# Optimization experiments

Measured on AMD Instinct MI355X. Metric: run time of the kernel, lower is better.

Reference implementation:

```python
import jax, jax.numpy as jnp
import numpy as np

HID = 2048        # hidden_size
STATE = 128       # ssm state size N
HEADS = 64
HEADDIM = 64
GROUPS = 1
K = 4             # conv kernel
INTER = 4096      # expand * hidden_size == HEADS * HEADDIM
CONV_DIM = INTER + 2 * GROUPS * STATE   # 4352
PROJ = INTER + CONV_DIM + HEADS         # 8512
EPS = 1e-5


def setup_inputs() -> dict:
    ks = jax.random.split(jax.random.key(0), 8)
    hidden_states = jax.random.normal(ks[0], (2, 2048, HID), dtype=jnp.float32)
    norm_weight = jnp.ones((HID,), jnp.float32)
    in_proj_w = jax.random.normal(ks[1], (PROJ, HID), jnp.float32) * 0.02
    conv_w = jax.random.normal(ks[2], (CONV_DIM, 1, K), jnp.float32) * 0.1
    conv_b = jax.random.normal(ks[3], (CONV_DIM,), jnp.float32) * 0.02
    dt_bias = jax.random.normal(ks[4], (HEADS,), jnp.float32) * 0.5
    A_log = jnp.log(jnp.arange(1, HEADS + 1, dtype=jnp.float32))
    D = jnp.ones((HEADS,), jnp.float32)
    gate_norm_weight = jnp.ones((INTER,), jnp.float32)
    out_proj_w = jax.random.normal(ks[5], (HID, INTER), jnp.float32) * 0.02
    return {"hidden_states": hidden_states, "norm_weight": norm_weight,
            "in_proj_w": in_proj_w, "conv_w": conv_w, "conv_b": conv_b,
            "dt_bias": dt_bias, "A_log": A_log, "D": D,
            "gate_norm_weight": gate_norm_weight, "out_proj_w": out_proj_w}


def _rmsnorm(x, w, eps):
    v = jnp.mean(jnp.square(x.astype(jnp.float32)), axis=-1, keepdims=True)
    return (x * jax.lax.rsqrt(v + eps)) * w


def _mamba2_block(hidden_states, norm_weight, in_proj_w, conv_w, conv_b,
                  dt_bias, A_log, D, gate_norm_weight, out_proj_w):
    b, s, _ = hidden_states.shape
    residual = hidden_states.astype(jnp.float32)  # residual_in_fp32
    x = _rmsnorm(hidden_states, norm_weight, EPS)

    proj = x @ in_proj_w.T                                  # [b,s,PROJ]
    gate, xBC, dt = jnp.split(proj, [INTER, INTER + CONV_DIM], axis=-1)

    # causal depthwise conv1d over channels, then SiLU
    xBC_t = jnp.swapaxes(xBC, 1, 2)                          # [b,C,s]
    conv = jax.lax.conv_general_dilated(
        xBC_t, conv_w, window_strides=(1,), padding=[(K - 1, 0)],
        dimension_numbers=("NCH", "OIH", "NCH"), feature_group_count=CONV_DIM)
    xBC = jax.nn.silu(jnp.swapaxes(conv + conv_b[None, :, None], 1, 2))

    xs, B, C = jnp.split(xBC, [INTER, INTER + GROUPS * STATE], axis=-1)
    hg = HEADS // GROUPS
    xs = xs.reshape(b, s, GROUPS, hg, HEADDIM)
    B = B.reshape(b, s, GROUPS, STATE)
    C = C.reshape(b, s, GROUPS, STATE)

    dt = jax.nn.softplus(dt + dt_bias).reshape(b, s, GROUPS, hg)  # [b,s,g,hg]
    A = -jnp.exp(A_log).reshape(GROUPS, hg)
    dA = jnp.exp(dt * A)                                     # [b,s,g,hg]
    dtx = dt[..., None] * xs                                  # [b,s,g,hg,p]

    def step(state, inp):
        dA_t, dtx_t, B_t, C_t = inp
        # state: [b,g,hg,p,n]
        state = state * dA_t[..., None, None] + jnp.einsum("bghp,bgn->bghpn", dtx_t, B_t)
        y_t = jnp.einsum("bghpn,bgn->bghp", state, C_t)
        return state, y_t

    mv = lambda a: jnp.moveaxis(a, 1, 0)  # time-major for scan
    state0 = jnp.zeros((b, GROUPS, hg, HEADDIM, STATE), jnp.float32)
    _, y = jax.lax.scan(step, state0, (mv(dA), mv(dtx), mv(B), mv(C)))
    y = jnp.moveaxis(y, 0, 1)                                 # [b,s,g,hg,p]
    y = y + D.reshape(GROUPS, hg)[..., None] * xs             # skip term
    y = y.reshape(b, s, INTER)

    # gated RMSNorm then output projection
    y = _rmsnorm(y * jax.nn.silu(gate), gate_norm_weight, EPS)
    out = y @ out_proj_w.T
    return residual + out


def reference(hidden_states, norm_weight, in_proj_w, conv_w, conv_b,
              dt_bias, A_log, D, gate_norm_weight, out_proj_w):
    return _mamba2_block(hidden_states, norm_weight, in_proj_w, conv_w, conv_b,
                         dt_bias, A_log, D, gate_norm_weight, out_proj_w)
```

## Files before the change

### kernel.cpp

```cpp
#include <hip/hip_runtime.h>
#include <math.h>

#define HID      2048
#define STATE    128
#define HEADS    64
#define HEADDIM  64
#define INTER    4096
#define CONV_DIM 4352
#define PROJ     8512
#define NBATCH   2
#define SEQ      2048
#define BS       (NBATCH*SEQ)
#define EPS      1e-5f
#define YN_COL   4160

typedef __attribute__((ext_vector_type(8))) short short8;
typedef __attribute__((ext_vector_type(4))) float f32x4;

__device__ inline unsigned short f2bf(float f) {
  union { float f; unsigned int u; } v; v.f = f;
  unsigned int r = v.u + 0x7fffu + ((v.u >> 16) & 1u);
  return (unsigned short)(r >> 16);
}
__device__ inline float bf2f(unsigned short b) {
  union { unsigned int u; float f; } v; v.u = ((unsigned int)b) << 16;
  return v.f;
}

__global__ __launch_bounds__(256)
void cast_bf16_kernel(const float4* __restrict__ src, ushort4* __restrict__ dst, int n4) {
  int i = blockIdx.x * 256 + threadIdx.x;
  if (i >= n4) return;
  float4 v = src[i];
  ushort4 o;
  o.x = f2bf(v.x); o.y = f2bf(v.y); o.z = f2bf(v.z); o.w = f2bf(v.w);
  dst[i] = o;
}

__global__ __launch_bounds__(256)
void rmsnorm_in_kernel(const float* __restrict__ x, const float* __restrict__ w,
                       unsigned short* __restrict__ xn) {
  int row = blockIdx.x;
  int t = threadIdx.x;
  const float* xr = x + (size_t)row * HID;
  float4 a = ((const float4*)xr)[t];
  float4 b = ((const float4*)xr)[t + 256];
  float ss = a.x*a.x + a.y*a.y + a.z*a.z + a.w*a.w
           + b.x*b.x + b.y*b.y + b.z*b.z + b.w*b.w;
  for (int o = 32; o > 0; o >>= 1) ss += __shfl_down(ss, o);
  __shared__ float red[4];
  __shared__ float scl;
  if ((t & 63) == 0) red[t >> 6] = ss;
  __syncthreads();
  if (t == 0) scl = rsqrtf((red[0]+red[1]+red[2]+red[3]) / (float)HID + EPS);
  __syncthreads();
  float s = scl;
  float4 w0 = ((const float4*)w)[t];
  float4 w1 = ((const float4*)w)[t + 256];
  ushort4 o0, o1;
  o0.x = f2bf(a.x*s*w0.x); o0.y = f2bf(a.y*s*w0.y); o0.z = f2bf(a.z*s*w0.z); o0.w = f2bf(a.w*s*w0.w);
  o1.x = f2bf(b.x*s*w1.x); o1.y = f2bf(b.y*s*w1.y); o1.z = f2bf(b.z*s*w1.z); o1.w = f2bf(b.w*s*w1.w);
  ushort4* dst = (ushort4*)(xn + (size_t)row * HID);
  dst[t] = o0;
  dst[t + 256] = o1;
}


__device__ __forceinline__ void stage_half(const unsigned short* __restrict__ G, int ld,
                                           int row0, int rmax, int kt,
                                           unsigned short* lbase, int half, int t) {
  const int w = t >> 6;
#pragma unroll
  for (int it = 0; it < 2; ++it) {
    int id = it * 512 + t;
    int rl = id >> 3;
    int sl = id & 7;
    int grow = row0 + half * 128 + rl;
    if (grow > rmax) grow = rmax;
    const unsigned short* g = G + (size_t)grow * ld + kt * 64 + ((sl ^ (rl & 7)) << 3);
    unsigned short* l = lbase + half * (128 * 64) + (it * 512 + w * 64) * 8;
    __builtin_amdgcn_global_load_lds((const __attribute__((address_space(1))) void*)g,
                                     (__attribute__((address_space(3))) void*)l, 16, 0, 0);
  }
}

#define VMW2 asm volatile("s_waitcnt vmcnt(2)" ::: "memory")

#define PHASE(BUF, MH, NH, RA, RB, STG, VMW_)                                        \
  {                                                                                  \
    const unsigned short* bufA = lds + (BUF)*24576;                                  \
    const unsigned short* bufB = lds + (BUF)*24576 + 16384;                          \
    if (RA) {                                                                        \
      _Pragma("unroll")                                                              \
      for (int ml = 0; ml < 2; ++ml) {                                               \
        _Pragma("unroll")                                                            \
        for (int kk = 0; kk < 2; ++kk) {                                             \
          const int r = wr*64 + (MH)*32 + ml*16 + tq;                                \
          aR[ml][kk] = *(const short8*)(bufA + r*64 + (((kk<<2)|quad)^(r&7))*8);     \
        }                                                                            \
      }                                                                              \
    }                                                                                \
    if (RB) {                                                                        \
      _Pragma("unroll")                                                              \
      for (int nl = 0; nl < 2; ++nl) {                                               \
        _Pragma("unroll")                                                            \
        for (int kk = 0; kk < 2; ++kk) {                                             \
          const int r = wc*64 + (NH)*32 + nl*16 + tq;                                \
          bR[NH][nl][kk] = *(const short8*)(bufB + r*64 + (((kk<<2)|quad)^(r&7))*8); \
        }                                                                            \
      }                                                                              \
    }                                                                                \
    STG;                                                                             \
    __builtin_amdgcn_s_barrier();                                                    \
    asm volatile("s_waitcnt lgkmcnt(0)" ::: "memory");                               \
    __builtin_amdgcn_sched_barrier(0);                                               \
    __builtin_amdgcn_s_setprio(1);                                                   \
    _Pragma("unroll")                                                                \
    for (int ml = 0; ml < 2; ++ml) {                                                 \
      _Pragma("unroll")                                                              \
      for (int nl = 0; nl < 2; ++nl) {                                               \
        _Pragma("unroll")                                                            \
        for (int kk = 0; kk < 2; ++kk) {                                             \
          acc[(MH)*2+ml][(NH)*2+nl] = __builtin_amdgcn_mfma_f32_16x16x32_bf16(       \
              aR[ml][kk], bR[NH][nl][kk], acc[(MH)*2+ml][(NH)*2+nl], 0, 0, 0);       \
        }                                                                            \
      }                                                                              \
    }                                                                                \
    __builtin_amdgcn_s_setprio(0);                                                   \
    VMW_;                                                                            \
    __builtin_amdgcn_s_barrier();                                                    \
  }

__global__ __launch_bounds__(512, 1)
void gemm128n_kernel(const unsigned short* __restrict__ A, int lda,
                     const unsigned short* __restrict__ B,
                     float* __restrict__ Cf, unsigned short* __restrict__ Cb, int ldc,
                     int M, int N, int Kd, const float* __restrict__ residual) {
  __shared__ unsigned short lds[49152];
  const int t = threadIdx.x;
  const int lane = t & 63;
  const int quad = lane >> 4;
  const int tq = lane & 15;
  const int w = t >> 6;
  const int wr = w >> 1;
  const int wc = w & 1;

  const int Mtiles = M >> 8;
  const int Ntiles = (N + 127) >> 7;
  const int nwg = (int)gridDim.x;
  const int cpx = nwg >> 3;
  const int bid = (int)blockIdx.x;
  const int sw = (bid & 7) * cpx + (bid >> 3);
  const int NBfull = Ntiles & ~7;
  int m0, n0;
  if (sw < Mtiles * NBfull) {
    int brick = sw >> 5;
    int inner = sw & 31;
    int bm = brick % (Mtiles >> 2);
    int bn = brick / (Mtiles >> 2);
    m0 = (bm * 4 + (inner & 3)) << 8;
    n0 = (bn * 8 + (inner >> 2)) << 7;
  } else {
    int r = sw - Mtiles * NBfull;
    m0 = (r % Mtiles) << 8;
    n0 = (NBfull + r / Mtiles) << 7;
  }

  f32x4 acc[4][4];
#pragma unroll
  for (int i = 0; i < 4; ++i)
#pragma unroll
    for (int j = 0; j < 4; ++j) acc[i][j] = (f32x4){0.f, 0.f, 0.f, 0.f};

  short8 aR[2][2];
  short8 bR[2][2][2];

  unsigned short* A0 = lds;
  unsigned short* B0 = lds + 16384;
  unsigned short* A1 = lds + 24576;
  unsigned short* B1 = lds + 24576 + 16384;

  const int kIters = Kd >> 6;
  const int nIter  = kIters >> 1;

  stage_half(A, lda, m0, M - 1, 0, A0, 0, t);
  stage_half(A, lda, m0, M - 1, 0, A0, 1, t);
  stage_half(B, Kd,  n0, N - 1, 0, B0, 0, t);
  stage_half(A, lda, m0, M - 1, 1, A1, 0, t);
  VMW2;
  __builtin_amdgcn_s_barrier();

  for (int i = 0; i < nIter; ++i) {
    const int k1 = 2 * i + 1;
    int k2 = 2 * i + 2; if (k2 > kIters - 1) k2 = kIters - 1;
    int k3 = 2 * i + 3; if (k3 > kIters - 1) k3 = kIters - 1;
    PHASE(0, 0, 0, 1, 1, stage_half(A, lda, m0, M - 1, k1, A1, 1, t), ((void)0))
    PHASE(0, 0, 1, 0, 1, stage_half(B, Kd,  n0, N - 1, k1, B1, 0, t), ((void)0))
    PHASE(0, 1, 1, 1, 0, ((void)0), ((void)0))
    PHASE(0, 1, 0, 0, 0, stage_half(A, lda, m0, M - 1, k2, A0, 0, t), VMW2)
    PHASE(1, 0, 0, 1, 1, stage_half(A, lda, m0, M - 1, k2, A0, 1, t), ((void)0))
    PHASE(1, 0, 1, 0, 1, stage_half(B, Kd,  n0, N - 1, k2, B0, 0, t), ((void)0))
    PHASE(1, 1, 1, 1, 0, ((void)0), ((void)0))
    PHASE(1, 1, 0, 0, 0, stage_half(A, lda, m0, M - 1, k3, A1, 0, t), VMW2)
  }
  asm volatile("s_waitcnt vmcnt(0)" ::: "memory");

#pragma unroll
  for (int mf = 0; mf < 4; ++mf) {
    const int rowb = m0 + wr * 64 + mf * 16 + quad * 4;
#pragma unroll
    for (int nf = 0; nf < 4; ++nf) {
      const int col = n0 + wc * 64 + nf * 16 + tq;
      if (col < N) {
        if (Cb) {
#pragma unroll
          for (int r = 0; r < 4; ++r)
            Cb[(size_t)(rowb + r) * ldc + col] = f2bf(acc[mf][nf][r]);
        } else {
#pragma unroll
          for (int r = 0; r < 4; ++r) {
            size_t idx = (size_t)(rowb + r) * N + col;
            float v = acc[mf][nf][r];
            if (residual) v += residual[idx];
            Cf[idx] = v;
          }
        }
      }
    }
  }
}

#define CONV_BC 128
#define CONV_BS 64
#define CXS 136

__global__ __launch_bounds__(256)
void conv_dt_kernel(const unsigned short* __restrict__ proj, const float* __restrict__ cw,
                    const float* __restrict__ cb, const float* __restrict__ dtb,
                    const float* __restrict__ A_log,
                    unsigned short* __restrict__ convo, float2* __restrict__ dts) {
  const int NCB = CONV_DIM / CONV_BC;
  const int NCONVB = NCB * (BS / CONV_BS);
  int blk = blockIdx.x;
  int t = threadIdx.x;
  if (blk < NCONVB) {
    __shared__ unsigned short xs[67 * CXS];
    int cblk = blk % NCB;
    int rblk = blk / NCB;
    int ch0 = cblk * CONV_BC;
    int rs0 = rblk * CONV_BS;
    int s0 = rs0 & (SEQ - 1);
    const int c8 = t & 15;
    const int co = c8 * 8;
    float cwr[4][8], cbr[8];
#pragma unroll
    for (int e = 0; e < 8; e++) {
      cbr[e] = cb[ch0 + co + e];
#pragma unroll
      for (int k = 0; k < 4; k++) cwr[k][e] = cw[(ch0 + co + e) * 4 + k];
    }
    for (int i = t; i < 67 * 16; i += 256) {
      int row = i >> 4, sl = i & 15;
      short8 v;
      if (s0 == 0 && row < 3) v = (short8){0,0,0,0,0,0,0,0};
      else v = *(const short8*)&proj[(size_t)(rs0 - 3 + row) * PROJ + INTER + ch0 + sl * 8];
      *(short8*)&xs[row * CXS + sl * 8] = v;
    }
    __syncthreads();
#pragma unroll
    for (int it = 0; it < 4; ++it) {
      int r = (t >> 4) + it * 16;
      float acc[8];
#pragma unroll
      for (int e = 0; e < 8; e++) acc[e] = cbr[e];
#pragma unroll
      for (int k = 0; k < 4; k++) {
        short8 v = *(const short8*)&xs[(r + k) * CXS + co];
#pragma unroll
        for (int e = 0; e < 8; e++) acc[e] += bf2f((unsigned short)v[e]) * cwr[k][e];
      }
      short8 o;
#pragma unroll
      for (int e = 0; e < 8; e++) {
        float a = acc[e];
        o[e] = (short)f2bf(a / (1.f + expf(-a)));
      }
      *(short8*)&convo[(size_t)(rs0 + r) * CONV_DIM + ch0 + co] = o;
    }
  } else {
    int k = (blk - NCONVB) * 256 + t;
    if (k < BS * HEADS) {
      int h  = k & 63;
      int rs = k >> 6;
      float x = bf2f(proj[(size_t)rs * PROJ + INTER + CONV_DIM + h]) + dtb[h];
      float dt = (x > 20.f) ? x : log1pf(expf(x));
      float Ah = -expf(A_log[h]);
      dts[k] = make_float2(dt, dt * Ah);
    }
  }
}

#define LCH 64
#define CST 136
#define TST 72

__global__ __launch_bounds__(512)
void ssd_scan_kernel(const unsigned short* __restrict__ convo, const float2* __restrict__ dts,
                     unsigned short* __restrict__ yp) {
  __shared__ unsigned short Cst[64 * CST];
  __shared__ unsigned short Bst[64 * CST];
  __shared__ unsigned short Btt[128 * TST];
  __shared__ unsigned short xtT[32 * TST];
  __shared__ unsigned short Msh[64 * TST];
  __shared__ unsigned short Sb[2][32 * CST];
  __shared__ float dtaL[64], dtvL[64];

  const int ph = blockIdx.x & 1;
  const int h  = (blockIdx.x >> 1) & 63;
  const int b  = blockIdx.x >> 7;
  const int t  = threadIdx.x;
  const int wv = t >> 6;
  const int lane = t & 63;
  const int quad = lane >> 4;
  const int tq   = lane & 15;
  const size_t row0 = (size_t)b * SEQ;
  const int xcol = h * 64 + ph * 32;

  for (int i = t; i < 32 * CST; i += 512) Sb[0][i] = 0;

  f32x4 s_acc[4];
#pragma unroll
  for (int c = 0; c < 4; c++) s_acc[c] = (f32x4){0.f, 0.f, 0.f, 0.f};
  const int pt  = wv & 1;
  const int ntb = ((wv >> 1) & 1) * 4;

  short8 vb_r[2], vc_r[2]; ushort4 vx_r; float2 dv_r = make_float2(0.f, 0.f);
  {
#pragma unroll
    for (int it = 0; it < 2; ++it) {
      int id = t + 512 * it;
      int row = id >> 4, cc = id & 15;
      size_t g = (row0 + row) * CONV_DIM + INTER;
      vb_r[it] = *(const short8*)&convo[g + cc * 8];
      vc_r[it] = *(const short8*)&convo[g + STATE + cc * 8];
    }
    int row = t >> 3, c = t & 7;
    vx_r = *(const ushort4*)&convo[(row0 + row) * CONV_DIM + xcol + c * 4];
    if (t < 64) dv_r = dts[((row0 + t) << 6) + h];
  }

  int pp = 0;
  for (int c0 = 0; c0 < SEQ; c0 += LCH, pp ^= 1) {
    __syncthreads();
#pragma unroll
    for (int it = 0; it < 2; ++it) {
      int id = t + 512 * it;
      int row = id >> 4, cc = id & 15;
      *(short8*)&Bst[row * CST + cc * 8] = vb_r[it];
      *(short8*)&Cst[row * CST + cc * 8] = vc_r[it];
#pragma unroll
      for (int e = 0; e < 8; e++)
        Btt[(cc * 8 + e) * TST + row] = (unsigned short)vb_r[it][e];
    }
    {
      int row = t >> 3, c = t & 7;
      xtT[(c * 4 + 0) * TST + row] = vx_r.x;
      xtT[(c * 4 + 1) * TST + row] = vx_r.y;
      xtT[(c * 4 + 2) * TST + row] = vx_r.z;
      xtT[(c * 4 + 3) * TST + row] = vx_r.w;
    }
    if (t < 64) { dtvL[t] = dv_r.x; dtaL[t] = dv_r.y; }
    __syncthreads();

    if (c0 + LCH < SEQ) {
#pragma unroll
      for (int it = 0; it < 2; ++it) {
        int id = t + 512 * it;
        int row = id >> 4, cc = id & 15;
        size_t g = (row0 + c0 + LCH + row) * CONV_DIM + INTER;
        vb_r[it] = *(const short8*)&convo[g + cc * 8];
        vc_r[it] = *(const short8*)&convo[g + STATE + cc * 8];
      }
      int row = t >> 3, c = t & 7;
      vx_r = *(const ushort4*)&convo[(row0 + c0 + LCH + row) * CONV_DIM + xcol + c * 4];
      if (t < 64) dv_r = dts[((row0 + c0 + LCH + t) << 6) + h];
    }

    float v = dtaL[lane];
#pragma unroll
    for (int off = 1; off < 64; off <<= 1) {
      float u = __shfl_up(v, off);
      if (lane >= off) v += u;
    }
    float tot = __shfl(v, 63);

    if (wv < 4) {
      short8 afC[4];
#pragma unroll
      for (int kt = 0; kt < 4; kt++)
        afC[kt] = *(const short8*)&Cst[(16 * wv + tq) * CST + kt * 32 + quad * 8];
      f32x4 g_acc[4];
#pragma unroll
      for (int nj = 0; nj < 4; nj++) g_acc[nj] = (f32x4){0.f, 0.f, 0.f, 0.f};
#pragma unroll
      for (int kt = 0; kt < 4; kt++) {
#pragma unroll
        for (int nj = 0; nj < 4; nj++) {
          short8 bfr = *(const short8*)&Bst[(16 * nj + tq) * CST + kt * 32 + quad * 8];
          g_acc[nj] = __builtin_amdgcn_mfma_f32_16x16x32_bf16(afC[kt], bfr, g_acc[nj], 0, 0, 0);
        }
      }
      float ci[4], pex[4];
#pragma unroll
      for (int r = 0; r < 4; r++) {
        ci[r] = __shfl(v, 16 * wv + quad * 4 + r);
        pex[r] = expf(ci[r]);
      }
#pragma unroll
      for (int nj = 0; nj < 4; nj++) {
        int j = 16 * nj + tq;
        float cj = __shfl(v, j);
        float dj = dtvL[j];
#pragma unroll
        for (int r = 0; r < 4; r++) {
          int i = 16 * wv + quad * 4 + r;
          float val = (j <= i) ? g_acc[nj][r] * expf(ci[r] - cj) * dj : 0.f;
          Msh[i * TST + j] = f2bf(val);
        }
      }
      f32x4 yac[2];
      yac[0] = (f32x4){0.f, 0.f, 0.f, 0.f};
      yac[1] = (f32x4){0.f, 0.f, 0.f, 0.f};
#pragma unroll
      for (int kt = 0; kt < 4; kt++) {
#pragma unroll
        for (int np = 0; np < 2; np++) {
          short8 bs = *(const short8*)&Sb[pp][(16 * np + tq) * CST + kt * 32 + quad * 8];
          yac[np] = __builtin_amdgcn_mfma_f32_16x16x32_bf16(afC[kt], bs, yac[np], 0, 0, 0);
        }
      }
#pragma unroll
      for (int np = 0; np < 2; np++)
#pragma unroll
        for (int r = 0; r < 4; r++) yac[np][r] *= pex[r];
#pragma unroll
      for (int kt2 = 0; kt2 < 2; kt2++) {
        short8 am = *(const short8*)&Msh[(16 * wv + tq) * TST + kt2 * 32 + quad * 8];
#pragma unroll
        for (int np = 0; np < 2; np++) {
          short8 bx = *(const short8*)&xtT[(16 * np + tq) * TST + kt2 * 32 + quad * 8];
          yac[np] = __builtin_amdgcn_mfma_f32_16x16x32_bf16(am, bx, yac[np], 0, 0, 0);
        }
      }
#pragma unroll
      for (int np = 0; np < 2; np++) {
#pragma unroll
        for (int r = 0; r < 4; r++) {
          int i = 16 * wv + quad * 4 + r;
          int p = ph * 32 + 16 * np + tq;
          yp[(row0 + c0 + i) * INTER + h * 64 + p] = f2bf(yac[np][r]);
        }
      }
    } else {
      float ptot = expf(tot);
      short8 ax[2];
#pragma unroll
      for (int kt2 = 0; kt2 < 2; kt2++) {
        short8 xv = *(const short8*)&xtT[(16 * pt + tq) * TST + kt2 * 32 + quad * 8];
#pragma unroll
        for (int e = 0; e < 8; e++) {
          int j = kt2 * 32 + quad * 8 + e;
          float cj = __shfl(v, j);
          float wj = expf(tot - cj) * dtvL[j];
          ax[kt2][e] = (short)f2bf(bf2f((unsigned short)xv[e]) * wj);
        }
      }
#pragma unroll
      for (int c = 0; c < 4; c++)
#pragma unroll
        for (int r = 0; r < 4; r++) s_acc[c][r] *= ptot;
#pragma unroll
      for (int kt2 = 0; kt2 < 2; kt2++) {
#pragma unroll
        for (int c = 0; c < 4; c++) {
          short8 bb = *(const short8*)&Btt[(16 * (ntb + c) + tq) * TST + kt2 * 32 + quad * 8];
          s_acc[c] = __builtin_amdgcn_mfma_f32_16x16x32_bf16(ax[kt2], bb, s_acc[c], 0, 0, 0);
        }
      }
#pragma unroll
      for (int c = 0; c < 4; c++)
#pragma unroll
        for (int r = 0; r < 4; r++) {
          int p = 16 * pt + quad * 4 + r;
          int n = 16 * (ntb + c) + tq;
          Sb[pp ^ 1][p * CST + n] = f2bf(s_acc[c][r]);
        }
    }
  }
}

__global__ __launch_bounds__(256)
void gated_norm_kernel(const unsigned short* __restrict__ yp,
                       const unsigned short* __restrict__ convo, const unsigned short* __restrict__ proj,
                       const float* __restrict__ Dv, const float* __restrict__ gnw,
                       unsigned short* __restrict__ yn) {
  int row = blockIdx.x;
  int t = threadIdx.x;
  __shared__ float red[4];
  __shared__ float scl;
  size_t yo = (size_t)row * INTER;
  size_t co = (size_t)row * CONV_DIM;
  size_t po = (size_t)row * PROJ;
  float vv[16];
  float ss = 0.f;
#pragma unroll
  for (int c = 0; c < 4; c++) {
    int i = t * 4 + c * 1024;
    ushort4 y0 = *(const ushort4*)&yp[yo + i];
    ushort4 xs = *(const ushort4*)&convo[co + i];
    ushort4 g  = *(const ushort4*)&proj[po + i];
    float Dh = Dv[i >> 6];
    float yv[4] = { bf2f(y0.x) + Dh * bf2f(xs.x),
                    bf2f(y0.y) + Dh * bf2f(xs.y),
                    bf2f(y0.z) + Dh * bf2f(xs.z),
                    bf2f(y0.w) + Dh * bf2f(xs.w) };
    float gv[4] = { bf2f(g.x), bf2f(g.y), bf2f(g.z), bf2f(g.w) };
#pragma unroll
    for (int k = 0; k < 4; k++) {
      float val = yv[k] * (gv[k] / (1.f + expf(-gv[k])));
      vv[c * 4 + k] = val;
      ss += val * val;
    }
  }
  for (int o = 32; o > 0; o >>= 1) ss += __shfl_down(ss, o);
  if ((t & 63) == 0) red[t >> 6] = ss;
  __syncthreads();
  if (t == 0) scl = rsqrtf((red[0]+red[1]+red[2]+red[3]) / (float)INTER + EPS);
  __syncthreads();
  float s = scl;
#pragma unroll
  for (int c = 0; c < 4; c++) {
    int i = t * 4 + c * 1024;
    ushort4 o;
    o.x = f2bf(vv[c*4+0] * s * gnw[i + 0]);
    o.y = f2bf(vv[c*4+1] * s * gnw[i + 1]);
    o.z = f2bf(vv[c*4+2] * s * gnw[i + 2]);
    o.w = f2bf(vv[c*4+3] * s * gnw[i + 3]);
    *(ushort4*)&yn[po + i] = o;
  }
}

extern "C" void kernel_launch(void* const* d_in, const int* in_sizes, int n_in,
                              void* d_out, int out_size, void* d_ws, size_t ws_size,
                              hipStream_t stream) {
  const float* hidden  = (const float*)d_in[0];
  const float* norm_w  = (const float*)d_in[1];
  const float* w1      = (const float*)d_in[2];
  const float* convw   = (const float*)d_in[3];
  const float* convb   = (const float*)d_in[4];
  const float* dt_bias = (const float*)d_in[5];
  const float* A_log   = (const float*)d_in[6];
  const float* Dv      = (const float*)d_in[7];
  const float* gnw     = (const float*)d_in[8];
  const float* w2      = (const float*)d_in[9];
  float* out = (float*)d_out;

  char* ws = (char*)d_ws;
  size_t off = 0;
  auto alloc = [&](size_t bytes) {
    void* p = ws + off;
    off += (bytes + 255) & ~(size_t)255;
    return p;
  };
  unsigned short* XN  = (unsigned short*)alloc((size_t)BS * HID * 2);
  unsigned short* W1B = (unsigned short*)alloc((size_t)PROJ * HID * 2);
  unsigned short* W2B = (unsigned short*)alloc((size_t)HID * INTER * 2);
  unsigned short* PRJ = (unsigned short*)alloc((size_t)BS * PROJ * 2);
  unsigned short* CVO = (unsigned short*)alloc((size_t)BS * CONV_DIM * 2);
  float2*         DTS = (float2*)alloc((size_t)BS * HEADS * 8);
  unsigned short* YP  = XN;
  unsigned short* YN  = PRJ + YN_COL;
  if (off > ws_size) return;
  (void)in_sizes; (void)n_in; (void)out_size;

  int n1 = PROJ * HID / 4;
  cast_bf16_kernel<<<(n1 + 255) / 256, 256, 0, stream>>>((const float4*)w1, (ushort4*)W1B, n1);
  int n2 = HID * INTER / 4;
  cast_bf16_kernel<<<(n2 + 255) / 256, 256, 0, stream>>>((const float4*)w2, (ushort4*)W2B, n2);

  rmsnorm_in_kernel<<<BS, 256, 0, stream>>>(hidden, norm_w, XN);

  gemm128n_kernel<<<dim3((BS / 256) * ((PROJ + 127) / 128)), 512, 0, stream>>>(
      XN, HID, W1B, nullptr, PRJ, PROJ, BS, PROJ, HID, nullptr);

  conv_dt_kernel<<<(CONV_DIM / CONV_BC) * (BS / CONV_BS) + (BS * HEADS) / 256, 256, 0, stream>>>(
      PRJ, convw, convb, dt_bias, A_log, CVO, DTS);

  ssd_scan_kernel<<<256, 512, 0, stream>>>(CVO, DTS, YP);

  gated_norm_kernel<<<BS, 256, 0, stream>>>(YP, CVO, PRJ, Dv, gnw, YN);

  gemm128n_kernel<<<dim3((BS / 256) * (HID / 128)), 512, 0, stream>>>(
      YN, PROJ, W2B, out, nullptr, HID, BS, HID, INTER, hidden);
}
```

Before: 599.4 us.

## Shrink GEMM tile to 128x128 with 256 threads and two blocks per CU

Replaces the 256x128 tile, 512-thread GEMM with a 128x128 tile, 256-thread kernel using half the LDS, so two workgroups can share a CU. The staging schedule is reworked: A and B are each loaded as two 64-row halves spread across the eight phases, with a deeper vmcnt wait, and the block swizzle now groups 8x8 tiles. This aims to raise occupancy and latency hiding and to give more workgroups for load balance. The cost is less data reuse per tile and more global and L2 traffic per FLOP.

```diff
diff --git a/kernel.cpp b/kernel.cpp
--- a/kernel.cpp
+++ b/kernel.cpp
@@ -66,30 +66,30 @@
 }
 
 
-__device__ __forceinline__ void stage_half(const unsigned short* __restrict__ G, int ld,
-                                           int row0, int rmax, int kt,
-                                           unsigned short* lbase, int half, int t) {
+__device__ __forceinline__ void stage_half64(const unsigned short* __restrict__ G, int ld,
+                                             int row0, int rmax, int kt,
+                                             unsigned short* lbase, int half, int t) {
   const int w = t >> 6;
 #pragma unroll
   for (int it = 0; it < 2; ++it) {
-    int id = it * 512 + t;
+    int id = it * 256 + t;
     int rl = id >> 3;
     int sl = id & 7;
-    int grow = row0 + half * 128 + rl;
+    int grow = row0 + half * 64 + rl;
     if (grow > rmax) grow = rmax;
     const unsigned short* g = G + (size_t)grow * ld + kt * 64 + ((sl ^ (rl & 7)) << 3);
-    unsigned short* l = lbase + half * (128 * 64) + (it * 512 + w * 64) * 8;
+    unsigned short* l = lbase + half * (64 * 64) + (it * 256 + w * 64) * 8;
     __builtin_amdgcn_global_load_lds((const __attribute__((address_space(1))) void*)g,
                                      (__attribute__((address_space(3))) void*)l, 16, 0, 0);
   }
 }
 
-#define VMW2 asm volatile("s_waitcnt vmcnt(2)" ::: "memory")
+#define VMW4 asm volatile("s_waitcnt vmcnt(4)" ::: "memory")
 
 #define PHASE(BUF, MH, NH, RA, RB, STG, VMW_)                                        \
   {                                                                                  \
-    const unsigned short* bufA = lds + (BUF)*24576;                                  \
-    const unsigned short* bufB = lds + (BUF)*24576 + 16384;                          \
+    const unsigned short* bufA = lds + (BUF)*16384;                                  \
+    const unsigned short* bufB = lds + (BUF)*16384 + 8192;                           \
     if (RA) {                                                                        \
       _Pragma("unroll")                                                              \
       for (int ml = 0; ml < 2; ++ml) {                                               \
@@ -131,12 +131,12 @@
     __builtin_amdgcn_s_barrier();                                                    \
   }
 
-__global__ __launch_bounds__(512, 1)
-void gemm128n_kernel(const unsigned short* __restrict__ A, int lda,
-                     const unsigned short* __restrict__ B,
-                     float* __restrict__ Cf, unsigned short* __restrict__ Cb, int ldc,
-                     int M, int N, int Kd, const float* __restrict__ residual) {
-  __shared__ unsigned short lds[49152];
+__global__ __launch_bounds__(256, 2)
+void gemm128_kernel(const unsigned short* __restrict__ A, int lda,
+                    const unsigned short* __restrict__ B,
+                    float* __restrict__ Cf, unsigned short* __restrict__ Cb, int ldc,
+                    int M, int N, int Kd, const float* __restrict__ residual) {
+  __shared__ unsigned short lds[32768];
   const int t = threadIdx.x;
   const int lane = t & 63;
   const int quad = lane >> 4;
@@ -145,7 +145,7 @@
   const int wr = w >> 1;
   const int wc = w & 1;
 
-  const int Mtiles = M >> 8;
+  const int Mtiles = M >> 7;
   const int Ntiles = (N + 127) >> 7;
   const int nwg = (int)gridDim.x;
   const int cpx = nwg >> 3;
@@ -154,15 +154,15 @@
   const int NBfull = Ntiles & ~7;
   int m0, n0;
   if (sw < Mtiles * NBfull) {
-    int brick = sw >> 5;
-    int inner = sw & 31;
-    int bm = brick % (Mtiles >> 2);
-    int bn = brick / (Mtiles >> 2);
-    m0 = (bm * 4 + (inner & 3)) << 8;
-    n0 = (bn * 8 + (inner >> 2)) << 7;
+    int brick = sw >> 6;
+    int inner = sw & 63;
+    int bm = brick % (Mtiles >> 3);
+    int bn = brick / (Mtiles >> 3);
+    m0 = (bm * 8 + (inner & 7)) << 7;
+    n0 = (bn * 8 + (inner >> 3)) << 7;
   } else {
     int r = sw - Mtiles * NBfull;
-    m0 = (r % Mtiles) << 8;
+    m0 = (r % Mtiles) << 7;
     n0 = (NBfull + r / Mtiles) << 7;
   }
 
@@ -176,32 +176,34 @@
   short8 bR[2][2][2];
 
   unsigned short* A0 = lds;
-  unsigned short* B0 = lds + 16384;
-  unsigned short* A1 = lds + 24576;
-  unsigned short* B1 = lds + 24576 + 16384;
+  unsigned short* B0 = lds + 8192;
+  unsigned short* A1 = lds + 16384;
+  unsigned short* B1 = lds + 24576;
 
   const int kIters = Kd >> 6;
   const int nIter  = kIters >> 1;
 
-  stage_half(A, lda, m0, M - 1, 0, A0, 0, t);
-  stage_half(A, lda, m0, M - 1, 0, A0, 1, t);
-  stage_half(B, Kd,  n0, N - 1, 0, B0, 0, t);
-  stage_half(A, lda, m0, M - 1, 1, A1, 0, t);
-  VMW2;
+  stage_half64(A, lda, m0, M - 1, 0, A0, 0, t);
+  stage_half64(A, lda, m0, M - 1, 0, A0, 1, t);
+  stage_half64(B, Kd,  n0, N - 1, 0, B0, 0, t);
+  stage_half64(B, Kd,  n0, N - 1, 0, B0, 1, t);
+  stage_half64(B, Kd,  n0, N - 1, 1, B1, 0, t);
+  stage_half64(B, Kd,  n0, N - 1, 1, B1, 1, t);
+  VMW4;
   __builtin_amdgcn_s_barrier();
 
   for (int i = 0; i < nIter; ++i) {
     const int k1 = 2 * i + 1;
     int k2 = 2 * i + 2; if (k2 > kIters - 1) k2 = kIters - 1;
     int k3 = 2 * i + 3; if (k3 > kIters - 1) k3 = kIters - 1;
-    PHASE(0, 0, 0, 1, 1, stage_half(A, lda, m0, M - 1, k1, A1, 1, t), ((void)0))
-    PHASE(0, 0, 1, 0, 1, stage_half(B, Kd,  n0, N - 1, k1, B1, 0, t), ((void)0))
-    PHASE(0, 1, 1, 1, 0, ((void)0), ((void)0))
-    PHASE(0, 1, 0, 0, 0, stage_half(A, lda, m0, M - 1, k2, A0, 0, t), VMW2)
-    PHASE(1, 0, 0, 1, 1, stage_half(A, lda, m0, M - 1, k2, A0, 1, t), ((void)0))
-    PHASE(1, 0, 1, 0, 1, stage_half(B, Kd,  n0, N - 1, k2, B0, 0, t), ((void)0))
-    PHASE(1, 1, 1, 1, 0, ((void)0), ((void)0))
-    PHASE(1, 1, 0, 0, 0, stage_half(A, lda, m0, M - 1, k3, A1, 0, t), VMW2)
+    PHASE(0, 0, 0, 1, 1, stage_half64(A, lda, m0, M - 1, k1, A1, 0, t), ((void)0))
+    PHASE(0, 0, 1, 0, 1, stage_half64(A, lda, m0, M - 1, k1, A1, 1, t), ((void)0))
+    PHASE(0, 1, 1, 1, 0, stage_half64(B, Kd,  n0, N - 1, k2, B0, 0, t), ((void)0))
+    PHASE(0, 1, 0, 0, 0, stage_half64(B, Kd,  n0, N - 1, k2, B0, 1, t), VMW4)
+    PHASE(1, 0, 0, 1, 1, stage_half64(A, lda, m0, M - 1, k2, A0, 0, t), ((void)0))
+    PHASE(1, 0, 1, 0, 1, stage_half64(A, lda, m0, M - 1, k2, A0, 1, t), ((void)0))
+    PHASE(1, 1, 1, 1, 0, stage_half64(B, Kd,  n0, N - 1, k3, B1, 0, t), ((void)0))
+    PHASE(1, 1, 0, 0, 0, stage_half64(B, Kd,  n0, N - 1, k3, B1, 1, t), VMW4)
   }
   asm volatile("s_waitcnt vmcnt(0)" ::: "memory");
 
@@ -590,7 +592,7 @@
 
   rmsnorm_in_kernel<<<BS, 256, 0, stream>>>(hidden, norm_w, XN);
 
-  gemm128n_kernel<<<dim3((BS / 256) * ((PROJ + 127) / 128)), 512, 0, stream>>>(
+  gemm128_kernel<<<dim3((BS / 128) * ((PROJ + 127) / 128)), 256, 0, stream>>>(
       XN, HID, W1B, nullptr, PRJ, PROJ, BS, PROJ, HID, nullptr);
 
   conv_dt_kernel<<<(CONV_DIM / CONV_BC) * (BS / CONV_BS) + (BS * HEADS) / 256, 256, 0, stream>>>(
@@ -600,6 +602,6 @@
 
   gated_norm_kernel<<<BS, 256, 0, stream>>>(YP, CVO, PRJ, Dv, gnw, YN);
 
-  gemm128n_kernel<<<dim3((BS / 256) * (HID / 128)), 512, 0, stream>>>(
+  gemm128_kernel<<<dim3((BS / 128) * (HID / 128)), 256, 0, stream>>>(
       YN, PROJ, W2B, out, nullptr, HID, BS, HID, INTER, hidden);
 }
```

Result: no change. 587.8 us (-1.9%).
